# Optimization experiments

Hardware: AMD Instinct MI355X
Metric: run time of the kernel (lower is better)

The kernel has to match this reference:

```python
import jax, jax.numpy as jnp
import numpy as np

EPS = 1e-5
NUM_GROUPS = 32


def setup_inputs() -> dict:
    key = jax.random.key(0)
    ks = jax.random.split(key, 4)
    b, c, h, w = 8, 512, 32, 32
    x = jax.random.normal(ks[0], (b, c, h, w), dtype=jnp.float32)
    gn_weight = jnp.ones((c,), dtype=jnp.float32)
    gn_bias = jnp.zeros((c,), dtype=jnp.float32)
    qkv_w = jax.random.normal(ks[1], (3 * c, c), dtype=jnp.float32) * (1.0 / np.sqrt(c))
    qkv_b = jnp.zeros((3 * c,), dtype=jnp.float32)
    proj_w = jax.random.normal(ks[2], (c, c), dtype=jnp.float32) * (1.0 / np.sqrt(c))
    proj_b = jnp.zeros((c,), dtype=jnp.float32)
    return {"x": x, "gn_weight": gn_weight, "gn_bias": gn_bias,
            "qkv_w": qkv_w, "qkv_b": qkv_b, "proj_w": proj_w, "proj_b": proj_b}


def _group_norm(x, weight, bias):
    b, c, h, w = x.shape
    xg = x.reshape(b, NUM_GROUPS, c // NUM_GROUPS, h, w)
    mean = xg.mean(axis=(2, 3, 4), keepdims=True)
    var = xg.var(axis=(2, 3, 4), keepdims=True)
    xn = ((xg - mean) * jax.lax.rsqrt(var + EPS)).reshape(b, c, h, w)
    return xn * weight[None, :, None, None] + bias[None, :, None, None]


def reference(x, gn_weight, gn_bias, qkv_w, qkv_b, proj_w, proj_b):
    b, c, h, w = x.shape
    scale = c ** (-0.5)
    xn = _group_norm(x, gn_weight, gn_bias)
    # 1x1 conv == per-pixel matmul over channels
    qkv = jnp.einsum('bchw,oc->bohw', xn, qkv_w) + qkv_b[None, :, None, None]
    q, k, v = jnp.split(qkv.reshape(b, 3 * c, h * w), 3, axis=1)  # each [b, c, N]
    attn = jax.nn.softmax(jnp.einsum('bci,bcj->bij', q, k) * scale, axis=-1)
    out = jnp.einsum('bij,bcj->bci', attn, v).reshape(b, c, h, w)
    proj = jnp.einsum('bchw,oc->bohw', out, proj_w) + proj_b[None, :, None, None]
    return x + proj
```

## Files before the change

### kernel.cpp

```cpp
#include <hip/hip_runtime.h>
#include <cmath>

constexpr int Bsz = 8, Cch = 512, NPIX = 1024;
constexpr int NG = 32, CPG = 16;

typedef __attribute__((ext_vector_type(4))) float f32x4;
typedef __attribute__((ext_vector_type(8))) short s16x8;

#define GLOBAL_AS __attribute__((address_space(1)))
#define LDS_AS __attribute__((address_space(3)))

__device__ inline short f2bf(float f) {
  union { float f; unsigned u; } c = {f};
  unsigned r = (c.u + 0x7fffu + ((c.u >> 16) & 1u)) >> 16;
  return (short)r;
}

__device__ inline float wave_reduce_sum(float v) {
#pragma unroll
  for (int off = 32; off > 0; off >>= 1) v += __shfl_xor(v, off, 64);
  return v;
}

__global__ __launch_bounds__(256) void prep_kernel(
    const float* __restrict__ x, const float* __restrict__ w,
    const float* __restrict__ bb, short* __restrict__ xnt,
    const float* __restrict__ in1, short* __restrict__ out1, int n1,
    const float* __restrict__ in2, short* __restrict__ out2, int n2) {
  __shared__ float sm[8];
  if (blockIdx.x >= 256) {
    const int i = ((blockIdx.x - 256) * 256 + threadIdx.x) * 4;
    const float* in = in1;
    short* out = out1;
    int j = i;
    if (i >= n1) { in = in2; out = out2; j = i - n1; }
    if (j + 3 < (i >= n1 ? n2 : n1)) {
      float4 v = *(const float4*)(in + j);
      short o[4] = {f2bf(v.x), f2bf(v.y), f2bf(v.z), f2bf(v.w)};
      *(uint2*)(out + j) = *(const uint2*)o;
    }
    return;
  }
  const int bg = blockIdx.x, b = bg >> 5, g = bg & 31;
  const float* xp = x + ((size_t)(b * Cch + g * CPG)) * NPIX;
  float s = 0.f, ss = 0.f;
  for (int i = threadIdx.x * 4; i < CPG * NPIX; i += 1024) {
    float4 v = *(const float4*)(xp + i);
    s += v.x + v.y + v.z + v.w;
    ss += v.x * v.x + v.y * v.y + v.z * v.z + v.w * v.w;
  }
  s = wave_reduce_sum(s);
  ss = wave_reduce_sum(ss);
  const int wv = threadIdx.x >> 6;
  if ((threadIdx.x & 63) == 0) { sm[wv] = s; sm[4 + wv] = ss; }
  __syncthreads();
  const float tsum = sm[0] + sm[1] + sm[2] + sm[3];
  const float tsq = sm[4] + sm[5] + sm[6] + sm[7];
  const float inv_n = 1.0f / (CPG * NPIX);
  const float mean = tsum * inv_n;
  const float rstd = rsqrtf(tsq * inv_n - mean * mean + 1e-5f);
  float wc[CPG], bc[CPG];
#pragma unroll
  for (int c = 0; c < CPG; ++c) {
    wc[c] = w[g * CPG + c] * rstd;
    bc[c] = bb[g * CPG + c] - mean * wc[c];
  }
  for (int p = threadIdx.x; p < NPIX; p += 256) {
    short ov[CPG];
#pragma unroll
    for (int c = 0; c < CPG; ++c)
      ov[c] = f2bf(xp[(size_t)c * NPIX + p] * wc[c] + bc[c]);
    short* op = xnt + ((size_t)(b * NPIX + p)) * Cch + g * CPG;
    *(uint4*)op = *(const uint4*)&ov[0];
    *(uint4*)(op + 8) = *(const uint4*)&ov[8];
  }
}

template <int BM, int BN, int EPI>
__global__ __launch_bounds__(256) void mfma_gemm(
    const short* __restrict__ A, const short* __restrict__ B, int K, int lda,
    int ldb, long sA, long sB, const float* __restrict__ bias, float alpha,
    void* __restrict__ Cp, long sC, int ldc, void* __restrict__ C2p, long sC2,
    const float* __restrict__ resid, long sR) {
  constexpr int FM = BM / 32, FN = BN / 32;
  constexpr int NA = BM / 64, NB = BN / 64;
  __shared__ __align__(16) short Asl[BM * 32];
  __shared__ __align__(16) short Bsl[BN * 32];
  const int t = threadIdx.x;
  const int lane = t & 63, wave = t >> 6;
  const int bz = blockIdx.z;
  const int m0 = blockIdx.y * BM, n0 = blockIdx.x * BN;
  A += sA * bz;
  B += sB * bz;

  const short* ga[NA];
  const short* gb[NB];
  short* la[NA];
  short* lb[NB];
#pragma unroll
  for (int i = 0; i < NA; ++i) {
    const int s = i * 256 + t;
    const int row = ((s >> 6) * 16) + (s & 15);
    const int q = (s >> 4) & 3;
    ga[i] = A + (size_t)(m0 + row) * lda + q * 8;
    la[i] = Asl + s * 8;
  }
#pragma unroll
  for (int i = 0; i < NB; ++i) {
    const int s = i * 256 + t;
    const int row = ((s >> 6) * 16) + (s & 15);
    const int q = (s >> 4) & 3;
    gb[i] = B + (size_t)(n0 + row) * ldb + q * 8;
    lb[i] = Bsl + s * 8;
  }

  f32x4 acc[FM][FN] = {};
  const int wm = wave & 1, wn = wave >> 1;

  for (int k0 = 0; k0 < K; k0 += 32) {
#pragma unroll
    for (int i = 0; i < NA; ++i) {
      __builtin_amdgcn_global_load_lds((const GLOBAL_AS void*)ga[i],
                                       (LDS_AS void*)la[i], 16, 0, 0);
      ga[i] += 32;
    }
#pragma unroll
    for (int i = 0; i < NB; ++i) {
      __builtin_amdgcn_global_load_lds((const GLOBAL_AS void*)gb[i],
                                       (LDS_AS void*)lb[i], 16, 0, 0);
      gb[i] += 32;
    }
    __syncthreads();
    s16x8 af[FM], bf[FN];
#pragma unroll
    for (int i = 0; i < FM; ++i)
      af[i] = *(const s16x8*)(Asl + (wm * FM + i) * 512 + lane * 8);
#pragma unroll
    for (int i = 0; i < FN; ++i)
      bf[i] = *(const s16x8*)(Bsl + (wn * FN + i) * 512 + lane * 8);
#pragma unroll
    for (int im = 0; im < FM; ++im)
#pragma unroll
      for (int in = 0; in < FN; ++in)
        acc[im][in] = __builtin_amdgcn_mfma_f32_16x16x32_bf16(
            af[im], bf[in], acc[im][in], 0, 0, 0);
    __syncthreads();
  }

  const int quad = lane >> 4, nn = lane & 15;
#pragma unroll
  for (int im = 0; im < FM; ++im) {
#pragma unroll
    for (int in = 0; in < FN; ++in) {
      const int m = m0 + (wm * FM + im) * 16 + quad * 4;
      const int n = n0 + (wn * FN + in) * 16 + nn;
      if (EPI == 0) {
        if (m0 < 1024) {
          short* Cq = (short*)Cp + sC * bz;
          short o[4];
#pragma unroll
          for (int r = 0; r < 4; ++r) o[r] = f2bf(acc[im][in][r] + bias[m + r]);
          *(uint2*)(Cq + (size_t)n * ldc + m) = *(const uint2*)o;
        } else {
          short* Cv = (short*)C2p + sC2 * bz;
#pragma unroll
          for (int r = 0; r < 4; ++r)
            Cv[(size_t)(m - 1024 + r) * ldc + n] =
                f2bf(acc[im][in][r] + bias[m + r]);
        }
      } else {
        float* Cf = (float*)Cp + sC * bz;
        const float* R = resid + sR * bz;
#pragma unroll
        for (int r = 0; r < 4; ++r)
          Cf[(size_t)(m + r) * ldc + n] =
              acc[im][in][r] + bias[m + r] + R[(size_t)(m + r) * ldc + n];
      }
    }
  }
}

__global__ __launch_bounds__(256, 2) void flash_kernel(
    const short* __restrict__ qkt,
    const short* __restrict__ vbuf,
    short* __restrict__ Ot) {
  __shared__ __align__(16) short Ksl[2][2048 * 8];
  __shared__ __align__(16) short Psl[2][2][16][40];
  __shared__ float lsum[2][2][16];
  const int t = threadIdx.x;
  const int lane = t & 63, wave = t >> 6;
  const int wm = wave & 1, wn = wave >> 1;
  const int nn = lane & 15, quad = lane >> 4;
  const int b = blockIdx.y;
  const int q0 = blockIdx.x * 32;
  const float scale = 0.044194173824159216f;

  s16x8 qf[16];
  {
    const short* qp =
        qkt + ((size_t)(b * 1024 + q0 + wm * 16 + nn)) * 1024 + quad * 8;
#pragma unroll
    for (int s = 0; s < 16; ++s) qf[s] = *(const s16x8*)(qp + s * 32);
  }

  const short* gk[8];
#pragma unroll
  for (int i = 0; i < 8; ++i) {
    const int cc = i * 256 + t;
    const int s = cc >> 7, h = (cc >> 6) & 1, ll = cc & 63;
    const int row = h * 16 + (ll & 15);
    const int k = s * 32 + ((ll >> 4) & 3) * 8;
    gk[i] = qkt + ((size_t)(b * 1024 + row)) * 1024 + 512 + k;
  }
  const short* vbase =
      vbuf + ((size_t)(b * 512 + wn * 256 + nn)) * 1024 + quad * 8;

  f32x4 acc_o[16] = {};
  float lp[4] = {0.f, 0.f, 0.f, 0.f};

#pragma unroll
  for (int i = 0; i < 8; ++i)
    __builtin_amdgcn_global_load_lds(
        (const GLOBAL_AS void*)gk[i],
        (LDS_AS void*)(&Ksl[0][0] + (i * 256 + t) * 8), 16, 0, 0);
  __syncthreads();

  for (int tile = 0; tile < 32; ++tile) {
    const int cur = tile & 1;
    if (tile < 31) {
#pragma unroll
      for (int i = 0; i < 8; ++i)
        __builtin_amdgcn_global_load_lds(
            (const GLOBAL_AS void*)(gk[i] + (size_t)(tile + 1) * 32 * 1024),
            (LDS_AS void*)(&Ksl[cur ^ 1][0] + (i * 256 + t) * 8), 16, 0, 0);
    }
    const short* vp = vbase + (size_t)tile * 32;
    s16x8 vf[16];
#pragma unroll
    for (int f = 0; f < 8; ++f)
      vf[f] = *(const s16x8*)(vp + (size_t)f * 16 * 1024);
    f32x4 s_acc = {};
#pragma unroll
    for (int s = 0; s < 16; ++s) {
      s16x8 kf = *(const s16x8*)(&Ksl[cur][0] + ((s * 2 + wn) * 64 + lane) * 8);
      s_acc = __builtin_amdgcn_mfma_f32_16x16x32_bf16(qf[s], kf, s_acc, 0, 0, 0);
    }
#pragma unroll
    for (int f = 8; f < 16; ++f)
      vf[f] = *(const s16x8*)(vp + (size_t)f * 16 * 1024);
#pragma unroll
    for (int r = 0; r < 4; ++r) {
      float e = __expf(s_acc[r] * scale);
      lp[r] += e;
      Psl[cur][wm][quad * 4 + r][wn * 16 + nn] = f2bf(e);
    }
    __syncthreads();
    s16x8 pa = *(const s16x8*)(&Psl[cur][wm][0][0] + nn * 40 + quad * 8);
#pragma unroll
    for (int f = 0; f < 16; ++f)
      acc_o[f] =
          __builtin_amdgcn_mfma_f32_16x16x32_bf16(pa, vf[f], acc_o[f], 0, 0, 0);
  }

#pragma unroll
  for (int off = 1; off < 16; off <<= 1)
#pragma unroll
    for (int r = 0; r < 4; ++r) lp[r] += __shfl_xor(lp[r], off, 64);
  if (nn == 0) {
#pragma unroll
    for (int r = 0; r < 4; ++r) lsum[wm][wn][quad * 4 + r] = lp[r];
  }
  __syncthreads();
  float inv[4];
#pragma unroll
  for (int r = 0; r < 4; ++r) {
    const int row = quad * 4 + r;
    inv[r] = 1.0f / (lsum[wm][0][row] + lsum[wm][1][row]);
  }
  short* op = Ot + ((size_t)(b * 1024 + q0 + wm * 16 + quad * 4)) * 512 +
              wn * 256 + nn;
#pragma unroll
  for (int f = 0; f < 16; ++f)
#pragma unroll
    for (int r = 0; r < 4; ++r)
      op[(size_t)r * 512 + f * 16] = f2bf(acc_o[f][r] * inv[r]);
}

extern "C" void kernel_launch(void* const* d_in, const int* in_sizes, int n_in,
                              void* d_out, int out_size, void* d_ws,
                              size_t ws_size, hipStream_t stream) {
  const float* x = (const float*)d_in[0];
  const float* gnw = (const float*)d_in[1];
  const float* gnb = (const float*)d_in[2];
  const float* qkvw = (const float*)d_in[3];
  const float* qkvb = (const float*)d_in[4];
  const float* projw = (const float*)d_in[5];
  const float* projb = (const float*)d_in[6];
  float* out = (float*)d_out;

  char* ws = (char*)d_ws;
  short* xnt = (short*)ws;
  short* qkt = (short*)(ws + (8ull << 20));
  short* vbuf = (short*)(ws + (24ull << 20));
  short* Ot = (short*)(ws + (32ull << 20));
  short* wq = (short*)(ws + (40ull << 20));
  short* wp = (short*)(ws + (42ull << 20));

  prep_kernel<<<1280, 256, 0, stream>>>(x, gnw, gnb, xnt, qkvw, wq, 1536 * 512,
                                        projw, wp, 512 * 512);

  mfma_gemm<128, 128, 0><<<dim3(8, 12, Bsz), 256, 0, stream>>>(
      wq, xnt, 512, 512, 512, 0L, 1024L * 512, qkvb, 1.0f, qkt, 1024L * 1024,
      1024, vbuf, 512L * 1024, nullptr, 0L);

  flash_kernel<<<dim3(32, Bsz), 256, 0, stream>>>(qkt, vbuf, Ot);

  mfma_gemm<64, 128, 3><<<dim3(8, 8, Bsz), 256, 0, stream>>>(
      wp, Ot, 512, 512, 512, 0L, 1024L * 512, projb, 1.0f, out, 512L * 1024,
      1024, nullptr, 0L, x, 512L * 1024);
}
```

Measured before the change: 228.0 us.

## Remap workgroups across XCDs, vectorize groupnorm writes, split flash QK accumulation

Block indices in the prep, GEMM and flash kernels are remapped so consecutive workgroups that share operands (the same batch or weight tiles) land on the same XCD, improving L2 locality on the multi-die MI355X. The groupnorm apply loop now reads float4 per channel and handles four pixels per thread instead of strided scalar loads. The flash kernel splits the QK^T MFMA chain into two independent accumulators to shorten the dependency chain. The remapping assumes the total workgroup count divides evenly by eight.

```diff
diff --git a/kernel.cpp b/kernel.cpp
--- a/kernel.cpp
+++ b/kernel.cpp
@@ -41,7 +41,8 @@
     }
     return;
   }
-  const int bg = blockIdx.x, b = bg >> 5, g = bg & 31;
+  const int bg = ((int)blockIdx.x & 7) * 32 + ((int)blockIdx.x >> 3);
+  const int b = bg >> 5, g = bg & 31;
   const float* xp = x + ((size_t)(b * Cch + g * CPG)) * NPIX;
   float s = 0.f, ss = 0.f;
   for (int i = threadIdx.x * 4; i < CPG * NPIX; i += 1024) {
@@ -65,14 +66,21 @@
     wc[c] = w[g * CPG + c] * rstd;
     bc[c] = bb[g * CPG + c] - mean * wc[c];
   }
-  for (int p = threadIdx.x; p < NPIX; p += 256) {
-    short ov[CPG];
-#pragma unroll
-    for (int c = 0; c < CPG; ++c)
-      ov[c] = f2bf(xp[(size_t)c * NPIX + p] * wc[c] + bc[c]);
-    short* op = xnt + ((size_t)(b * NPIX + p)) * Cch + g * CPG;
-    *(uint4*)op = *(const uint4*)&ov[0];
-    *(uint4*)(op + 8) = *(const uint4*)&ov[8];
+  const int p0 = threadIdx.x * 4;
+  short ov[4][CPG];
+#pragma unroll
+  for (int c = 0; c < CPG; ++c) {
+    float4 v = *(const float4*)(xp + (size_t)c * NPIX + p0);
+    ov[0][c] = f2bf(v.x * wc[c] + bc[c]);
+    ov[1][c] = f2bf(v.y * wc[c] + bc[c]);
+    ov[2][c] = f2bf(v.z * wc[c] + bc[c]);
+    ov[3][c] = f2bf(v.w * wc[c] + bc[c]);
+  }
+#pragma unroll
+  for (int j = 0; j < 4; ++j) {
+    short* op = xnt + ((size_t)(b * NPIX + p0 + j)) * Cch + g * CPG;
+    *(uint4*)op = *(const uint4*)&ov[j][0];
+    *(uint4*)(op + 8) = *(const uint4*)&ov[j][8];
   }
 }
 
@@ -88,8 +96,17 @@
   __shared__ __align__(16) short Bsl[BN * 32];
   const int t = threadIdx.x;
   const int lane = t & 63, wave = t >> 6;
-  const int bz = blockIdx.z;
-  const int m0 = blockIdx.y * BM, n0 = blockIdx.x * BN;
+
+  const int gx = gridDim.x, gy = gridDim.y;
+  const int nwg = gx * gy * (int)gridDim.z;
+  int flat = (int)blockIdx.x + gx * ((int)blockIdx.y + gy * (int)blockIdx.z);
+  flat = (flat & 7) * (nwg >> 3) + (flat >> 3);
+  const int bx = flat % gx;
+  const int rem = flat / gx;
+  const int by = rem % gy;
+  const int bz = rem / gy;
+
+  const int m0 = by * BM, n0 = bx * BN;
   A += sA * bz;
   B += sB * bz;
 
@@ -191,8 +208,10 @@
   const int lane = t & 63, wave = t >> 6;
   const int wm = wave & 1, wn = wave >> 1;
   const int nn = lane & 15, quad = lane >> 4;
-  const int b = blockIdx.y;
-  const int q0 = blockIdx.x * 32;
+  const int f = (int)blockIdx.x + 32 * (int)blockIdx.y;
+  const int flat = (f & 7) * 32 + (f >> 3);
+  const int b = flat >> 5;
+  const int q0 = (flat & 31) * 32;
   const float scale = 0.044194173824159216f;
 
   s16x8 qf[16];
@@ -237,17 +256,21 @@
     const short* vp = vbase + (size_t)tile * 32;
     s16x8 vf[16];
 #pragma unroll
-    for (int f = 0; f < 8; ++f)
-      vf[f] = *(const s16x8*)(vp + (size_t)f * 16 * 1024);
-    f32x4 s_acc = {};
-#pragma unroll
-    for (int s = 0; s < 16; ++s) {
-      s16x8 kf = *(const s16x8*)(&Ksl[cur][0] + ((s * 2 + wn) * 64 + lane) * 8);
-      s_acc = __builtin_amdgcn_mfma_f32_16x16x32_bf16(qf[s], kf, s_acc, 0, 0, 0);
-    }
-#pragma unroll
-    for (int f = 8; f < 16; ++f)
-      vf[f] = *(const s16x8*)(vp + (size_t)f * 16 * 1024);
+    for (int ff = 0; ff < 8; ++ff)
+      vf[ff] = *(const s16x8*)(vp + (size_t)ff * 16 * 1024);
+    f32x4 sa = {}, sb = {};
+#pragma unroll
+    for (int s = 0; s < 8; ++s) {
+      s16x8 kfa = *(const s16x8*)(&Ksl[cur][0] + ((s * 2 + wn) * 64 + lane) * 8);
+      s16x8 kfb =
+          *(const s16x8*)(&Ksl[cur][0] + (((s + 8) * 2 + wn) * 64 + lane) * 8);
+      sa = __builtin_amdgcn_mfma_f32_16x16x32_bf16(qf[s], kfa, sa, 0, 0, 0);
+      sb = __builtin_amdgcn_mfma_f32_16x16x32_bf16(qf[s + 8], kfb, sb, 0, 0, 0);
+    }
+    f32x4 s_acc = sa + sb;
+#pragma unroll
+    for (int ff = 8; ff < 16; ++ff)
+      vf[ff] = *(const s16x8*)(vp + (size_t)ff * 16 * 1024);
 #pragma unroll
     for (int r = 0; r < 4; ++r) {
       float e = __expf(s_acc[r] * scale);
@@ -257,9 +280,9 @@
     __syncthreads();
     s16x8 pa = *(const s16x8*)(&Psl[cur][wm][0][0] + nn * 40 + quad * 8);
 #pragma unroll
-    for (int f = 0; f < 16; ++f)
-      acc_o[f] =
-          __builtin_amdgcn_mfma_f32_16x16x32_bf16(pa, vf[f], acc_o[f], 0, 0, 0);
+    for (int ff = 0; ff < 16; ++ff)
+      acc_o[ff] =
+          __builtin_amdgcn_mfma_f32_16x16x32_bf16(pa, vf[ff], acc_o[ff], 0, 0, 0);
   }
 
 #pragma unroll
@@ -280,10 +303,10 @@
   short* op = Ot + ((size_t)(b * 1024 + q0 + wm * 16 + quad * 4)) * 512 +
               wn * 256 + nn;
 #pragma unroll
-  for (int f = 0; f < 16; ++f)
+  for (int ff = 0; ff < 16; ++ff)
 #pragma unroll
     for (int r = 0; r < 4; ++r)
-      op[(size_t)r * 512 + f * 16] = f2bf(acc_o[f][r] * inv[r]);
+      op[(size_t)r * 512 + ff * 16] = f2bf(acc_o[ff][r] * inv[r]);
 }
 
 extern "C" void kernel_launch(void* const* d_in, const int* in_sizes, int n_in,
@@ -313,7 +336,7 @@
       wq, xnt, 512, 512, 512, 0L, 1024L * 512, qkvb, 1.0f, qkt, 1024L * 1024,
       1024, vbuf, 512L * 1024, nullptr, 0L);
 
-  flash_kernel<<<dim3(32, Bsz), 256, 0, stream>>>(qkt, vbuf, Ot);
+  flash_kernel<<<dim3(32, 8), 256, 0, stream>>>(qkt, vbuf, Ot);
 
   mfma_gemm<64, 128, 3><<<dim3(8, 8, Bsz), 256, 0, stream>>>(
       wp, Ot, 512, 512, 512, 0L, 1024L * 512, projb, 1.0f, out, 512L * 1024,
```

Measured after the change: 226.0 us. No clear change (-0.9%).
